# Optimization experiments

Measured on AMD Instinct MI355X. Metric: run time of the kernel, lower is better.

Reference implementation:

```python
import jax, jax.numpy as jnp
from jax import lax
import numpy as np

B, T, N_OBS, M_STATE, HID = 64, 1024, 64, 64, 512


def setup_inputs() -> dict:
    key = jax.random.key(0)
    ks = jax.random.split(key, 9)
    # Stable state-transition matrix: scaled orthogonal so F^t does not blow up over T steps.
    A = np.asarray(jax.random.normal(ks[0], (M_STATE, M_STATE), dtype=jnp.float32))
    Q, _ = np.linalg.qr(A)
    F_mat = jnp.asarray(0.99 * Q, dtype=jnp.float32)
    s = 0.05
    return {
        "Y": jax.random.normal(ks[1], (B, T, N_OBS), dtype=jnp.float32),
        "x0_hat": jax.random.normal(ks[2], (B, M_STATE), dtype=jnp.float32),
        "F_mat": F_mat,
        "W_ih": s * jax.random.normal(ks[3], (3 * HID, N_OBS + M_STATE), dtype=jnp.float32),
        "W_hh": s * jax.random.normal(ks[4], (3 * HID, HID), dtype=jnp.float32),
        "b_ih": s * jax.random.normal(ks[5], (3 * HID,), dtype=jnp.float32),
        "b_hh": s * jax.random.normal(ks[6], (3 * HID,), dtype=jnp.float32),
        "fc_W": s * jax.random.normal(ks[7], (M_STATE, HID), dtype=jnp.float32),
        "fc_b": s * jax.random.normal(ks[8], (M_STATE,), dtype=jnp.float32),
    }


def _forward(Y, x0_hat, F_mat, W_ih, W_hh, b_ih, b_hh, fc_W, fc_b):
    Bb, Tt, _ = Y.shape
    H = W_hh.shape[1]

    # Prior linear recurrence: x_prior_t = F @ x_prior_{t-1}, x_prior_0 seeded by x0_hat.
    # NOTE: faithful to the source, the loop feeds x_prior (not the posterior) back in.
    def prior_step(x, _):
        x_new = x @ F_mat.T  # [B, m]
        return x_new, x_new

    _, X_prior = lax.scan(prior_step, x0_hat, None, length=Tt)  # [T, B, m]
    X_prior = jnp.transpose(X_prior, (1, 0, 2))  # [B, T, m]

    inp = jnp.concatenate([Y, X_prior], axis=-1)  # [B, T, n+m]

    # One big GEMM for the input projection of all gates over all timesteps.
    x_proj = inp @ W_ih.T + b_ih  # [B, T, 3H]

    def gru_step(h, xp):
        hp = h @ W_hh.T + b_hh  # [B, 3H]
        xr, xz, xn = jnp.split(xp, 3, axis=-1)
        hr, hz, hn = jnp.split(hp, 3, axis=-1)
        r = jax.nn.sigmoid(xr + hr)
        z = jax.nn.sigmoid(xz + hz)
        n = jnp.tanh(xn + r * hn)
        h_new = (1.0 - z) * n + z * h
        return h_new, h_new

    h0 = jnp.zeros((Bb, H), dtype=Y.dtype)
    _, outs = lax.scan(gru_step, h0, jnp.transpose(x_proj, (1, 0, 2)))  # [T, B, H]
    outs = jnp.transpose(outs, (1, 0, 2))  # [B, T, H]

    dX = outs @ fc_W.T + fc_b  # [B, T, m]
    return X_prior + dX


def reference(Y, x0_hat, F_mat, W_ih, W_hh, b_ih, b_hh, fc_W, fc_b):
    return _forward(Y, x0_hat, F_mat, W_ih, W_hh, b_ih, b_hh, fc_W, fc_b)
```

## Files before the change

kernel.cpp:

```cpp
#include <hip/hip_runtime.h>

typedef unsigned int u32;
typedef unsigned short u16;
typedef _Float16 half8 __attribute__((ext_vector_type(8)));
typedef float f32x4 __attribute__((ext_vector_type(4)));
typedef _Float16 h2t __attribute__((ext_vector_type(2)));

union H2U { u32 u; h2t h; u16 s[2]; };
union U128 { uint4 u; half8 h; };

#if defined(__has_builtin)
#if __has_builtin(__builtin_amdgcn_fdot2)
#define HAS_FDOT2 1
#endif
#endif

__device__ __forceinline__ float dot2f(u32 w, u32 x, float acc){
  H2U a, b; a.u = w; b.u = x;
#ifdef HAS_FDOT2
  return __builtin_amdgcn_fdot2(a.h, b.h, acc, false);
#else
  return acc + (float)a.h.x * (float)b.h.x + (float)a.h.y * (float)b.h.y;
#endif
}
__device__ __forceinline__ u32 packh2(float a, float b){
  H2U u; u.h.x = (_Float16)a; u.h.y = (_Float16)b; return u.u;
}
__device__ __forceinline__ u16 f16b(float x){
  union { _Float16 h; u16 u; } c; c.h = (_Float16)x; return c.u;
}
__device__ __forceinline__ float rcpf(float x){ return __builtin_amdgcn_rcpf(x); }
__device__ __forceinline__ float sigm(float x){ return rcpf(1.0f + __expf(-x)); }
__device__ __forceinline__ float sigm_slow(float x){ return 1.0f/(1.0f + __expf(-x)); }
__device__ __forceinline__ float tanh_f(float x){
  return fmaf(-2.0f, rcpf(1.0f + __expf(2.0f*x)), 1.0f);
}
__device__ __forceinline__ half8 pack8(float4 u, float4 v){
  half8 r;
  r[0]=(_Float16)u.x; r[1]=(_Float16)u.y; r[2]=(_Float16)u.z; r[3]=(_Float16)u.w;
  r[4]=(_Float16)v.x; r[5]=(_Float16)v.y; r[6]=(_Float16)v.z; r[7]=(_Float16)v.w;
  return r;
}

#define LDX4_SC(dst, base, off) \
  asm volatile("global_load_dwordx4 %0, %1, off offset:" #off " sc0 sc1" \
               : "=&v"(dst) : "v"(base) : "memory")
#define STX2_SC(base, v2) \
  asm volatile("global_store_dwordx2 %0, %1, off sc0 sc1" \
               :: "v"(base), "v"(v2) : "memory")
#define STDW_SC(base, val) \
  asm volatile("global_store_dword %0, %1, off sc0 sc1" \
               :: "v"(base), "v"(val) : "memory")
#define WAIT_VM0() asm volatile("s_waitcnt vmcnt(0)" ::: "memory")

#define T_STEPS 1024
#define NB 64
#define HID 512
#define G3 1536
#define NOBS 64
#define MST 64
#define KIN 128

#define OFF_WHHK 0
#define SZ_WHHK (G3*HID*2)
#define OFF_WIHK (OFF_WHHK + SZ_WHHK)
#define SZ_WIHK (G3*KIN*2)
#define OFF_FCK (OFF_WIHK + SZ_WIHK)
#define SZ_FCK (MST*HID*2)
#define OFF_FLG (OFF_FCK + SZ_FCK)
#define FLG_STRIDE 16
#define SZ_FLG (4*32*FLG_STRIDE*4)
#define OFF_HFULL (OFF_FLG + SZ_FLG + 4096)
#define SZ_HFULL ((size_t)T_STEPS*NB*HID*2)
#define WS_NEED (OFF_HFULL + SZ_HFULL)

__global__ __launch_bounds__(256) void prep2_kernel(
    const float* __restrict__ W_ih, const float* __restrict__ W_hh,
    const float* __restrict__ fc_W, char* __restrict__ ws){
  _Float16* whhk = (_Float16*)(ws + OFF_WHHK);
  _Float16* wihk = (_Float16*)(ws + OFF_WIHK);
  _Float16* fck  = (_Float16*)(ws + OFF_FCK);
  u32* flg       = (u32*)(ws + OFF_FLG);
  long idx = (long)blockIdx.x*256 + threadIdx.x;
  const long N1 = (long)G3*HID, N2 = (long)G3*KIN, N3 = (long)MST*HID;
  const long N4 = SZ_FLG/4;
  if (idx < N1) whhk[idx] = (_Float16)W_hh[idx];
  else if (idx < N1+N2) wihk[idx-N1] = (_Float16)W_ih[idx-N1];
  else if (idx < N1+N2+N3) fck[idx-N1-N2] = (_Float16)fc_W[idx-N1-N2];
  else if (idx < N1+N2+N3+N4) { u32* p = flg + (idx-N1-N2-N3); u32 z = 0; STDW_SC(p, z); }
}

__global__ __launch_bounds__(64) void xprior_kernel(
    const float* __restrict__ F, const float* __restrict__ x0,
    float* __restrict__ out){
  int b = blockIdx.x, i = threadIdx.x;
  __shared__ float xb[2][64];
  float f[64];
  #pragma unroll
  for (int j=0;j<64;j++) f[j] = F[i*64+j];
  xb[0][i] = x0[b*64+i];
  __syncthreads();
  float* o = out + (size_t)b*1024*64;
  for (int t=0;t<1024;t++){
    int cur = t & 1;
    float a0=0.f,a1=0.f,a2=0.f,a3=0.f;
    #pragma unroll
    for (int j=0;j<64;j+=4){
      a0 = fmaf(f[j+0], xb[cur][j+0], a0);
      a1 = fmaf(f[j+1], xb[cur][j+1], a1);
      a2 = fmaf(f[j+2], xb[cur][j+2], a2);
      a3 = fmaf(f[j+3], xb[cur][j+3], a3);
    }
    float a = (a0+a1)+(a2+a3);
    o[t*64+i] = a;
    xb[cur^1][i] = a;
    __syncthreads();
  }
}

__global__ __launch_bounds__(128, 1) void gru_pers3(
    const float* __restrict__ Y, const float* __restrict__ Xp,
    const float* __restrict__ b_ih, const float* __restrict__ b_hh,
    char* __restrict__ ws){
  const _Float16* whhk = (const _Float16*)(ws + OFF_WHHK);
  const _Float16* wihk = (const _Float16*)(ws + OFF_WIHK);
  u32* flags           = (u32*)(ws + OFF_FLG);
  _Float16* h_full     = (_Float16*)(ws + OFF_HFULL);

  const int blk = blockIdx.x;
  const int g = blk >> 5;
  const int m = blk & 31;
  const int tid = threadIdx.x;
  const int wv = tid >> 6;
  const int lane = tid & 63;
  const int lr = lane & 15, lk = lane >> 4;
  const int j = m*16 + lr;

  half8 BhR[8], BhZ[8], BhN[8], BxR[2], BxZ[2], BxN[2];
  #pragma unroll
  for (int c=0;c<8;c++){
    BhR[c] = *(const half8*)(whhk + ((size_t)(       j))*HID + wv*256 + c*32 + lk*8);
    BhZ[c] = *(const half8*)(whhk + ((size_t)(512  + j))*HID + wv*256 + c*32 + lk*8);
    BhN[c] = *(const half8*)(whhk + ((size_t)(1024 + j))*HID + wv*256 + c*32 + lk*8);
  }
  #pragma unroll
  for (int c=0;c<2;c++){
    BxR[c] = *(const half8*)(wihk + ((size_t)(       j))*KIN + wv*64 + c*32 + lk*8);
    BxZ[c] = *(const half8*)(wihk + ((size_t)(512  + j))*KIN + wv*64 + c*32 + lk*8);
    BxN[c] = *(const half8*)(wihk + ((size_t)(1024 + j))*KIN + wv*64 + c*32 + lk*8);
  }

  const int j4 = m*16 + lk*4;
  float bRv[4], bZv[4], bNXv[4], bNHv[4];
  #pragma unroll
  for (int r=0;r<4;r++){
    bRv[r]  = b_ih[j4+r]      + b_hh[j4+r];
    bZv[r]  = b_ih[512+j4+r]  + b_hh[512+j4+r];
    bNXv[r] = b_ih[1024+j4+r];
    bNHv[r] = b_hh[1024+j4+r];
  }

  const float* Arow = (wv==0 ? Y : Xp) + ((size_t)(g*16 + lr))*T_STEPS*64;

  u32* flg = flags + g*32*FLG_STRIDE;
  u32* myflag   = flg + m*FLG_STRIDE;
  u32* pollflag = flg + (wv*16 + (lane & 15))*FLG_STRIDE;

  float hold[4] = {0.f, 0.f, 0.f, 0.f};
  __shared__ f32x4 part[2][4][64];

  for (int t=0; t<T_STEPS; t++){
    const int s = t & 1;

    const float* asrc = Arow + (size_t)t*64;
    float4 i0 = *(const float4*)(asrc + lk*8);
    float4 i1 = *(const float4*)(asrc + lk*8 + 4);
    float4 i2 = *(const float4*)(asrc + 32 + lk*8);
    float4 i3 = *(const float4*)(asrc + 32 + lk*8 + 4);

    if (t > 0){
      u32 v;
      for(;;){
        asm volatile("global_load_dword %0, %1, off sc0 sc1\n\ts_waitcnt vmcnt(0)"
                     : "=&v"(v) : "v"(pollflag) : "memory");
        if (__all((int)(v >= (u32)t))) break;
      }
    }

    uint4 ah[8];
    if (t > 0){
      const _Float16* hb = h_full + ((size_t)(t-1)*NB + g*16 + lr)*HID + wv*256 + lk*8;
      LDX4_SC(ah[0], hb,   0); LDX4_SC(ah[1], hb,  64);
      LDX4_SC(ah[2], hb, 128); LDX4_SC(ah[3], hb, 192);
      LDX4_SC(ah[4], hb, 256); LDX4_SC(ah[5], hb, 320);
      LDX4_SC(ah[6], hb, 384); LDX4_SC(ah[7], hb, 448);
    }

    f32x4 aR={0,0,0,0}, aZ={0,0,0,0}, aNH={0,0,0,0}, aNX={0,0,0,0};
    {
      half8 A0 = pack8(i0,i1), A1 = pack8(i2,i3);
      aR  = __builtin_amdgcn_mfma_f32_16x16x32_f16(BxR[0], A0, aR, 0,0,0);
      aZ  = __builtin_amdgcn_mfma_f32_16x16x32_f16(BxZ[0], A0, aZ, 0,0,0);
      aNX = __builtin_amdgcn_mfma_f32_16x16x32_f16(BxN[0], A0, aNX,0,0,0);
      aR  = __builtin_amdgcn_mfma_f32_16x16x32_f16(BxR[1], A1, aR, 0,0,0);
      aZ  = __builtin_amdgcn_mfma_f32_16x16x32_f16(BxZ[1], A1, aZ, 0,0,0);
      aNX = __builtin_amdgcn_mfma_f32_16x16x32_f16(BxN[1], A1, aNX,0,0,0);
    }

    WAIT_VM0();
    __builtin_amdgcn_sched_barrier(0);

    if (t > 0){
      #pragma unroll
      for (int c=0;c<8;c++){
        U128 u; u.u = ah[c];
        half8 B = u.h;
        aR  = __builtin_amdgcn_mfma_f32_16x16x32_f16(BhR[c], B, aR, 0,0,0);
        aZ  = __builtin_amdgcn_mfma_f32_16x16x32_f16(BhZ[c], B, aZ, 0,0,0);
        aNH = __builtin_amdgcn_mfma_f32_16x16x32_f16(BhN[c], B, aNH,0,0,0);
      }
    }

    if (wv == 1){
      part[s][0][lane] = aR;  part[s][1][lane] = aZ;
      part[s][2][lane] = aNH; part[s][3][lane] = aNX;
    }
    __syncthreads();

    if (wv == 0){
      aR  += part[s][0][lane]; aZ  += part[s][1][lane];
      aNH += part[s][2][lane]; aNX += part[s][3][lane];
      float hn[4];
      #pragma unroll
      for (int r=0;r<4;r++){
        float rg = sigm(aR[r] + bRv[r]);
        float zg = sigm(aZ[r] + bZv[r]);
        float ng = tanh_f(aNX[r] + bNXv[r] + rg*(aNH[r] + bNHv[r]));
        hn[r] = (1.f - zg)*ng + zg*hold[r];
        hold[r] = hn[r];
      }
      _Float16* hw = h_full + ((size_t)t*NB + g*16 + lr)*HID + j4;
      uint2 qq = make_uint2(packh2(hn[0], hn[1]), packh2(hn[2], hn[3]));
      STX2_SC(hw, qq);
      WAIT_VM0();
      if (lane == 0){
        u32 tv = (u32)(t+1);
        STDW_SC(myflag, tv);
      }
    }
  }
}

__global__ __launch_bounds__(256) void fc_kernel(
    const float* __restrict__ fc_b, const char* __restrict__ ws,
    float* __restrict__ out){
  const _Float16* fck    = (const _Float16*)(ws + OFF_FCK);
  const _Float16* h_full = (const _Float16*)(ws + OFF_HFULL);
  int blk = blockIdx.x;
  int b  = blk >> 5;
  int t0 = (blk & 31) * 32;
  int tid = threadIdx.x, wv = tid >> 6, lane = tid & 63;
  int lr = lane & 15, lk = lane >> 4;
  int n = wv*16 + lr;
  half8 Bf[16];
  #pragma unroll
  for (int c=0;c<16;c++)
    Bf[c] = *(const half8*)(fck + (size_t)n*HID + c*32 + lk*8);
  float bias = fc_b[n];
  #pragma unroll
  for (int mt=0;mt<2;mt++){
    f32x4 C = {0.f,0.f,0.f,0.f};
    #pragma unroll
    for (int c=0;c<16;c++){
      half8 A = *(const half8*)(h_full + ((size_t)(t0+mt*16+lr)*NB + b)*HID + c*32 + lk*8);
      C = __builtin_amdgcn_mfma_f32_16x16x32_f16(A, Bf[c], C, 0,0,0);
    }
    #pragma unroll
    for (int r=0;r<4;r++){
      int trow = t0 + mt*16 + lk*4 + r;
      size_t o = ((size_t)b*T_STEPS + trow)*MST + n;
      out[o] = out[o] + bias + C[r];
    }
  }
}

#define NHH (3*128*512)
#define NIH (3*32*512)
#define NFC (8*16*64)

__global__ __launch_bounds__(256) void prep_kernel(
    const float* __restrict__ W_ih, const float* __restrict__ W_hh,
    const float* __restrict__ fc_W, uint2* __restrict__ whh_p,
    uint2* __restrict__ wih_p, uint2* __restrict__ wfc_p){
  int idx = blockIdx.x*256 + threadIdx.x;
  if (idx < NHH){
    int g = idx >> 16, rem = idx & 65535, k4 = rem >> 9, jj = rem & 511;
    const float* src = W_hh + (g*512 + jj)*512 + k4*4;
    whh_p[idx] = make_uint2(packh2(src[0],src[1]), packh2(src[2],src[3]));
  } else if (idx < NHH + NIH){
    int t = idx - NHH;
    int g = t >> 14, rem = t & 16383, k4 = rem >> 9, jj = rem & 511;
    const float* src = W_ih + (g*512 + jj)*128 + k4*4;
    wih_p[t] = make_uint2(packh2(src[0],src[1]), packh2(src[2],src[3]));
  } else {
    int t = idx - NHH - NIH;
    int ss = t >> 10, rem = t & 1023, k4 = rem >> 6, i = rem & 63;
    const float* src = fc_W + i*512 + ss*64 + k4*4;
    wfc_p[t] = make_uint2(packh2(src[0],src[1]), packh2(src[2],src[3]));
  }
}

__global__ __launch_bounds__(512) void gru_kernel(
    const float* __restrict__ Y, const float* __restrict__ b_ih,
    const float* __restrict__ b_hh, const float* __restrict__ fc_b,
    const uint2* __restrict__ WIH, const uint2* __restrict__ WHH,
    const uint2* __restrict__ WFC, float* __restrict__ out){
  int b = blockIdx.x, j = threadIdx.x;
  int ss = j >> 6, ii = j & 63;
  __shared__ u32 inp2[64];
  __shared__ float xp_lds[64];
  __shared__ u32 hbuf2[256];
  __shared__ float fcred[8][64];
  float br  = b_ih[j]      + b_hh[j];
  float bz  = b_ih[512+j]  + b_hh[512+j];
  float bxn = b_ih[1024+j];
  float bhn = b_hh[1024+j];
  float fb  = (j<64)? fc_b[j] : 0.f;
  float hreg = 0.f;
  if (j < 256) hbuf2[j] = 0u;
  const float* yb = Y   + (size_t)b*1024*64;
  float*       ob = out + (size_t)b*1024*64;
  for (int t=0;t<1024;t++){
    const float* yrow = yb + t*64;
    float*       orow = ob + t*64;
    if (j < 64){
      xp_lds[j] = orow[j];
      if (j < 32){
        float2 v = *(const float2*)(yrow + 2*j);
        inp2[j] = packh2(v.x, v.y);
      } else {
        float2 v = *(const float2*)(orow + 2*(j-32));
        inp2[j] = packh2(v.x, v.y);
      }
    }
    __syncthreads();
    float sr=br, sz=bz, sxn=bxn, shn=bhn;
    #pragma unroll 8
    for (int m=0;m<32;m++){
      uint2 wr = WIH[(m   )*512 + j];
      uint2 wz = WIH[(32+m)*512 + j];
      uint2 wn = WIH[(64+m)*512 + j];
      u32 x0 = inp2[2*m], x1 = inp2[2*m+1];
      sr  = dot2f(wr.x,x0,sr );  sr  = dot2f(wr.y,x1,sr );
      sz  = dot2f(wz.x,x0,sz );  sz  = dot2f(wz.y,x1,sz );
      sxn = dot2f(wn.x,x0,sxn);  sxn = dot2f(wn.y,x1,sxn);
    }
    #pragma unroll 8
    for (int m=0;m<128;m++){
      uint2 wr = WHH[(m     )*512 + j];
      uint2 wz = WHH[(128+m)*512 + j];
      uint2 wn = WHH[(256+m)*512 + j];
      u32 h0 = hbuf2[2*m], h1 = hbuf2[2*m+1];
      sr  = dot2f(wr.x,h0,sr );  sr  = dot2f(wr.y,h1,sr );
      sz  = dot2f(wz.x,h0,sz );  sz  = dot2f(wz.y,h1,sz );
      shn = dot2f(wn.x,h0,shn);  shn = dot2f(wn.y,h1,shn);
    }
    float r  = sigm_slow(sr);
    float zg = sigm_slow(sz);
    float ng = tanhf(sxn + r*shn);
    float hnew = (1.f - zg)*ng + zg*hreg;
    hreg = hnew;
    __syncthreads();
    ((u16*)hbuf2)[j] = f16b(hnew);
    __syncthreads();
    float p = 0.f;
    #pragma unroll
    for (int k4=0;k4<16;k4++){
      uint2 w2 = WFC[(ss*16 + k4)*64 + ii];
      u32 h0 = hbuf2[ss*32 + 2*k4], h1 = hbuf2[ss*32 + 2*k4 + 1];
      p = dot2f(w2.x,h0,p);  p = dot2f(w2.y,h1,p);
    }
    fcred[ss][ii] = p;
    __syncthreads();
    if (j < 64){
      float dx = fb + xp_lds[j];
      #pragma unroll
      for (int q=0;q<8;q++) dx += fcred[q][j];
      orow[j] = dx;
    }
  }
}

extern "C" void kernel_launch(void* const* d_in, const int* in_sizes, int n_in,
                              void* d_out, int out_size, void* d_ws, size_t ws_size,
                              hipStream_t stream){
  (void)in_sizes; (void)n_in; (void)out_size;
  const float* Y   = (const float*)d_in[0];
  const float* x0  = (const float*)d_in[1];
  const float* F   = (const float*)d_in[2];
  const float* Wih = (const float*)d_in[3];
  const float* Whh = (const float*)d_in[4];
  const float* bih = (const float*)d_in[5];
  const float* bhh = (const float*)d_in[6];
  const float* fcW = (const float*)d_in[7];
  const float* fcb = (const float*)d_in[8];
  float* out = (float*)d_out;

  if (ws_size >= (size_t)WS_NEED){
    char* ws = (char*)d_ws;
    prep2_kernel <<<3976, 256, 0, stream>>>(Wih, Whh, fcW, ws);
    xprior_kernel<<<  64,  64, 0, stream>>>(F, x0, out);
    gru_pers3    <<< 128, 128, 0, stream>>>(Y, out, bih, bhh, ws);
    fc_kernel    <<<2048, 256, 0, stream>>>(fcb, ws, out);
  } else {
    uint2* whh_p = (uint2*)d_ws;
    uint2* wih_p = (uint2*)((char*)d_ws + 1572864);
    uint2* wfc_p = (uint2*)((char*)d_ws + 1966080);
    prep_kernel  <<<992, 256, 0, stream>>>(Wih, Whh, fcW, whh_p, wih_p, wfc_p);
    xprior_kernel<<< 64,  64, 0, stream>>>(F, x0, out);
    gru_kernel   <<< 64, 512, 0, stream>>>(Y, bih, bhh, fcb, wih_p, whh_p, wfc_p, out);
  }
}
```

Baseline: 3.075 ms.

## Consolidate persistent GRU into 32 larger blocks with fewer cross-block flags

Each persistent GRU block now owns 64 hidden units with 8 waves, split into 4 column quarters times 2 K-halves, instead of 16 units with 2 waves. This gives 32 blocks instead of 128 and 8 flags per batch group instead of 32. Each wave now polls only 4 flags rather than 16, which cuts the cost of the per-step cross-block synchronisation. The trade-off is an extra block-wide barrier before the flag store, and fewer CUs are used.

Result: slower. 4.792 ms (+55.9%).

```diff
diff --git a/kernel.cpp b/kernel.cpp
--- a/kernel.cpp
+++ b/kernel.cpp
@@ -69,7 +69,7 @@
 #define SZ_FCK (MST*HID*2)
 #define OFF_FLG (OFF_FCK + SZ_FCK)
 #define FLG_STRIDE 16
-#define SZ_FLG (4*32*FLG_STRIDE*4)
+#define SZ_FLG (4*8*FLG_STRIDE*4)
 #define OFF_HFULL (OFF_FLG + SZ_FLG + 4096)
 #define SZ_HFULL ((size_t)T_STEPS*NB*HID*2)
 #define WS_NEED (OFF_HFULL + SZ_HFULL)
@@ -118,7 +118,7 @@
   }
 }
 
-__global__ __launch_bounds__(128, 1) void gru_pers3(
+__global__ __launch_bounds__(512, 1) void gru_pers8(
     const float* __restrict__ Y, const float* __restrict__ Xp,
     const float* __restrict__ b_ih, const float* __restrict__ b_hh,
     char* __restrict__ ws){
@@ -128,29 +128,32 @@
   _Float16* h_full     = (_Float16*)(ws + OFF_HFULL);
 
   const int blk = blockIdx.x;
-  const int g = blk >> 5;
-  const int m = blk & 31;
+  const int g = blk >> 3;
+  const int m = blk & 7;
   const int tid = threadIdx.x;
-  const int wv = tid >> 6;
+  const int w8 = tid >> 6;
+  const int kh = w8 & 1;
+  const int cq = w8 >> 1;
   const int lane = tid & 63;
   const int lr = lane & 15, lk = lane >> 4;
-  const int j = m*16 + lr;
+  const int jb = m*64 + cq*16;
+  const int j  = jb + lr;
 
   half8 BhR[8], BhZ[8], BhN[8], BxR[2], BxZ[2], BxN[2];
   #pragma unroll
   for (int c=0;c<8;c++){
-    BhR[c] = *(const half8*)(whhk + ((size_t)(       j))*HID + wv*256 + c*32 + lk*8);
-    BhZ[c] = *(const half8*)(whhk + ((size_t)(512  + j))*HID + wv*256 + c*32 + lk*8);
-    BhN[c] = *(const half8*)(whhk + ((size_t)(1024 + j))*HID + wv*256 + c*32 + lk*8);
+    BhR[c] = *(const half8*)(whhk + ((size_t)(       j))*HID + kh*256 + c*32 + lk*8);
+    BhZ[c] = *(const half8*)(whhk + ((size_t)(512  + j))*HID + kh*256 + c*32 + lk*8);
+    BhN[c] = *(const half8*)(whhk + ((size_t)(1024 + j))*HID + kh*256 + c*32 + lk*8);
   }
   #pragma unroll
   for (int c=0;c<2;c++){
-    BxR[c] = *(const half8*)(wihk + ((size_t)(       j))*KIN + wv*64 + c*32 + lk*8);
-    BxZ[c] = *(const half8*)(wihk + ((size_t)(512  + j))*KIN + wv*64 + c*32 + lk*8);
-    BxN[c] = *(const half8*)(wihk + ((size_t)(1024 + j))*KIN + wv*64 + c*32 + lk*8);
-  }
-
-  const int j4 = m*16 + lk*4;
+    BxR[c] = *(const half8*)(wihk + ((size_t)(       j))*KIN + kh*64 + c*32 + lk*8);
+    BxZ[c] = *(const half8*)(wihk + ((size_t)(512  + j))*KIN + kh*64 + c*32 + lk*8);
+    BxN[c] = *(const half8*)(wihk + ((size_t)(1024 + j))*KIN + kh*64 + c*32 + lk*8);
+  }
+
+  const int j4 = jb + lk*4;
   float bRv[4], bZv[4], bNXv[4], bNHv[4];
   #pragma unroll
   for (int r=0;r<4;r++){
@@ -160,14 +163,14 @@
     bNHv[r] = b_hh[1024+j4+r];
   }
 
-  const float* Arow = (wv==0 ? Y : Xp) + ((size_t)(g*16 + lr))*T_STEPS*64;
-
-  u32* flg = flags + g*32*FLG_STRIDE;
+  const float* Arow = (kh==0 ? Y : Xp) + ((size_t)(g*16 + lr))*T_STEPS*64;
+
+  u32* flg = flags + g*8*FLG_STRIDE;
   u32* myflag   = flg + m*FLG_STRIDE;
-  u32* pollflag = flg + (wv*16 + (lane & 15))*FLG_STRIDE;
+  u32* pollflag = flg + (kh*4 + (lane & 3))*FLG_STRIDE;
 
   float hold[4] = {0.f, 0.f, 0.f, 0.f};
-  __shared__ f32x4 part[2][4][64];
+  __shared__ f32x4 part[2][4][4][64];
 
   for (int t=0; t<T_STEPS; t++){
     const int s = t & 1;
@@ -189,7 +192,7 @@
 
     uint4 ah[8];
     if (t > 0){
-      const _Float16* hb = h_full + ((size_t)(t-1)*NB + g*16 + lr)*HID + wv*256 + lk*8;
+      const _Float16* hb = h_full + ((size_t)(t-1)*NB + g*16 + lr)*HID + kh*256 + lk*8;
       LDX4_SC(ah[0], hb,   0); LDX4_SC(ah[1], hb,  64);
       LDX4_SC(ah[2], hb, 128); LDX4_SC(ah[3], hb, 192);
       LDX4_SC(ah[4], hb, 256); LDX4_SC(ah[5], hb, 320);
@@ -221,15 +224,15 @@
       }
     }
 
-    if (wv == 1){
-      part[s][0][lane] = aR;  part[s][1][lane] = aZ;
-      part[s][2][lane] = aNH; part[s][3][lane] = aNX;
-    }
-    __syncthreads();
-
-    if (wv == 0){
-      aR  += part[s][0][lane]; aZ  += part[s][1][lane];
-      aNH += part[s][2][lane]; aNX += part[s][3][lane];
+    if (kh == 1){
+      part[s][cq][0][lane] = aR;  part[s][cq][1][lane] = aZ;
+      part[s][cq][2][lane] = aNH; part[s][cq][3][lane] = aNX;
+    }
+    __syncthreads();
+
+    if (kh == 0){
+      aR  += part[s][cq][0][lane]; aZ  += part[s][cq][1][lane];
+      aNH += part[s][cq][2][lane]; aNX += part[s][cq][3][lane];
       float hn[4];
       #pragma unroll
       for (int r=0;r<4;r++){
@@ -243,10 +246,12 @@
       uint2 qq = make_uint2(packh2(hn[0], hn[1]), packh2(hn[2], hn[3]));
       STX2_SC(hw, qq);
       WAIT_VM0();
-      if (lane == 0){
-        u32 tv = (u32)(t+1);
-        STDW_SC(myflag, tv);
-      }
+    }
+    __syncthreads();
+
+    if (tid == 0){
+      u32 tv = (u32)(t+1);
+      STDW_SC(myflag, tv);
     }
   }
 }
@@ -408,9 +413,9 @@
 
   if (ws_size >= (size_t)WS_NEED){
     char* ws = (char*)d_ws;
-    prep2_kernel <<<3976, 256, 0, stream>>>(Wih, Whh, fcW, ws);
+    prep2_kernel <<<3971, 256, 0, stream>>>(Wih, Whh, fcW, ws);
     xprior_kernel<<<  64,  64, 0, stream>>>(F, x0, out);
-    gru_pers3    <<< 128, 128, 0, stream>>>(Y, out, bih, bhh, ws);
+    gru_pers8    <<<  32, 512, 0, stream>>>(Y, out, bih, bhh, ws);
     fc_kernel    <<<2048, 256, 0, stream>>>(fcb, ws, out);
   } else {
     uint2* whh_p = (uint2*)d_ws;
```
